# Kernel optimization log

Hardware: AMD Instinct MI355X
Metric: run time of the kernel (lower is better)

The kernel has to match this reference:

```python
import jax, jax.numpy as jnp
import numpy as np

TAU = 2.0      # spikingjelly MultiStepLIFNode default tau
VTH = 1.0      # default v_threshold
ALPHA = 4.0    # default Sigmoid surrogate alpha
EPS = 1e-5     # BatchNorm eps

# --- STE sign for binarized conv weights (Binarize.apply, det mode, scale=1) ---
@jax.custom_vjp
def ste_sign(x):
    return jnp.sign(x)

def _ss_fwd(x):
    return jnp.sign(x), None

def _ss_bwd(_, g):
    return (g,)

ste_sign.defvjp(_ss_fwd, _ss_bwd)

# --- Heaviside spike with sigmoid surrogate gradient ---
@jax.custom_vjp
def spike_fn(x):
    return (x >= 0.0).astype(x.dtype)

def _sp_fwd(x):
    return (x >= 0.0).astype(x.dtype), x

def _sp_bwd(x, g):
    s = jax.nn.sigmoid(ALPHA * x)
    return (g * ALPHA * s * (1.0 - s),)

spike_fn.defvjp(_sp_fwd, _sp_bwd)

def lif(x):
    # x: [T,B,C,H,W]; LIF with v_reset=None (soft reset), decay_input=True,
    # detach_reset=True (stop_gradient on the reset term).
    def step(v, xt):
        v = v + (xt - v) / TAU
        s = spike_fn(v - VTH)
        v = v - jax.lax.stop_gradient(s) * VTH
        return v, s
    v0 = jnp.zeros_like(x[0])
    _, spikes = jax.lax.scan(step, v0, x)
    return spikes

def conv3x3(x, w, groups=1):
    # x: [N,C,H,W], w: [O, C//groups, 3, 3], stride 1, pad 1
    return jax.lax.conv_general_dilated(
        x, w, window_strides=(1, 1), padding=((1, 1), (1, 1)),
        dimension_numbers=('NCHW', 'OIHW', 'NCHW'),
        feature_group_count=groups)

def setup_inputs() -> dict:
    key = jax.random.key(0)
    k1, k2, k3 = jax.random.split(key, 3)
    x = jax.random.normal(k1, (4, 8, 256, 64, 64), dtype=jnp.float32)
    w1 = jax.random.normal(k2, (192, 256, 3, 3), dtype=jnp.float32) * 0.05
    gamma = jnp.ones((192,), dtype=jnp.float32)
    beta = jnp.zeros((192,), dtype=jnp.float32)
    w2 = jax.random.normal(k3, (320, 48, 3, 3), dtype=jnp.float32) * 0.05
    return {'x': x, 'w1': w1, 'gamma': gamma, 'beta': beta, 'w2': w2}

def reference(x, w1, gamma, beta, w2):
    T, B, C, H, W = x.shape
    s = lif(x).reshape(T * B, C, H, W)          # spikes, flatten(0,1)
    y = conv3x3(s, w1)                          # conv1 (bias=False)
    # BatchNorm2d in training mode: batch stats over (N,H,W), biased var
    mean = y.mean(axis=(0, 2, 3))
    var = y.var(axis=(0, 2, 3))
    yb = (y - mean[None, :, None, None]) * jax.lax.rsqrt(var + EPS)[None, :, None, None]
    yb = yb * gamma[None, :, None, None] + beta[None, :, None, None]
    hidden = yb.shape[1]
    x1 = yb.reshape(T, B, hidden, H, W)
    z = conv3x3(yb, ste_sign(w2), groups=4)     # binarized-weight conv, groups=4
    x2 = z.reshape(T, B, -1, H, W)
    return jnp.concatenate((x1, x2), axis=2)    # [T,B,output_size,H,W]
```

## Files before the change

### kernel.cpp

```cpp
#include <hip/hip_runtime.h>

typedef __bf16 bf16x8 __attribute__((ext_vector_type(8)));
typedef float f32x4 __attribute__((ext_vector_type(4)));

#define DEV static __device__ __forceinline__

DEV ushort f2bf(float f) {
  unsigned u = __builtin_bit_cast(unsigned, f);
  u = (u + 0x7FFFu + ((u >> 16) & 1u)) >> 16;
  return (ushort)u;
}
DEV float bf2f(ushort h) {
  unsigned u = ((unsigned)h) << 16;
  return __builtin_bit_cast(float, u);
}
DEV void gll16(const void* g, void* l) {
  __builtin_amdgcn_global_load_lds((const __attribute__((address_space(1))) void*)g,
                                   (__attribute__((address_space(3))) void*)l, 16, 0, 0);
}

#define Y_OFF      71368704ull
#define WR1_OFF    121700352ull
#define WR2_OFF    122585088ull
#define STATS_OFF  122953728ull
#define ZERO_OFF   122955264ull
#define PART_OFF   122959360ull

DEV void border_px(int p, int& h, int& w) {
  if (p < 66)       { h = 0;       w = p; }
  else if (p < 132) { h = 65;      w = p - 66; }
  else if (p < 196) { h = p - 131; w = 0; }
  else              { h = p - 195; w = 65; }
}
__global__ void halo1_kernel(ushort* __restrict__ S) {
  const int idx = blockIdx.x * 256 + threadIdx.x;
  const int n = idx / 16640, r = idx % 16640;
  const int p = r >> 6, c4 = r & 63;
  int h, w; border_px(p, h, w);
  ushort4 z; z.x = 0; z.y = 0; z.z = 0; z.w = 0;
  *(ushort4*)&S[((size_t)((n * 66 + h) * 66 + w) << 8) + c4 * 4] = z;
}
__global__ void halo2_kernel(ushort* __restrict__ Yb) {
  const int idx = blockIdx.x * 256 + threadIdx.x;
  const int n = idx / 12480, r = idx % 12480;
  const int p = r / 48, c4 = r % 48;
  int h, w; border_px(p, h, w);
  ushort4 z; z.x = 0; z.y = 0; z.z = 0; z.w = 0;
  *(ushort4*)&Yb[(size_t)((n * 66 + h) * 66 + w) * 192 + c4 * 4] = z;
}

__global__ __launch_bounds__(256) void lif_kernel(const float* __restrict__ x,
                                                  ushort* __restrict__ S) {
  const int bi = blockIdx.x;
  const int jq = bi >> 9;
  const int b  = (bi >> 6) & 7;
  const int h  = bi & 63;
  const int tid = threadIdx.x;
  const int w0 = (tid & 15) << 2;
  const int cg = (tid >> 4) + (jq << 4);
  const int c0 = cg << 2;

  float v[4][4];
#pragma unroll
  for (int a = 0; a < 4; ++a)
#pragma unroll
    for (int k = 0; k < 4; ++k) v[a][k] = 0.f;

#pragma unroll
  for (int t = 0; t < 4; ++t) {
    const int n = t * 8 + b;
    ushort sp[4][4];
#pragma unroll
    for (int a = 0; a < 4; ++a) {
      const float4 xv = *(const float4*)(x + ((size_t)(n * 256 + c0 + a) << 12) + (h << 6) + w0);
      const float xa[4] = {xv.x, xv.y, xv.z, xv.w};
#pragma unroll
      for (int k = 0; k < 4; ++k) {
        v[a][k] += (xa[k] - v[a][k]) * 0.5f;
        const bool s = v[a][k] >= 1.0f;
        sp[a][k] = s ? (ushort)0x3F80 : (ushort)0;
        v[a][k] -= s ? 1.0f : 0.0f;
      }
    }
#pragma unroll
    for (int k = 0; k < 4; ++k) {
      ushort4 o4; o4.x = sp[0][k]; o4.y = sp[1][k]; o4.z = sp[2][k]; o4.w = sp[3][k];
      *(ushort4*)(S + ((size_t)((n * 66 + h + 1) * 66 + (w0 + k + 1)) << 8) + c0) = o4;
    }
  }
}

__global__ void prep_w1_kernel(const float* __restrict__ w1, ushort* __restrict__ Wr1) {
  const int idx = blockIdx.x * 256 + threadIdx.x;
  const int pos = idx / 49152, r = idx % 49152;
  const int o = r >> 8, c = r & 255;
  Wr1[idx] = f2bf(w1[(o * 256 + c) * 9 + pos]);
}
__global__ void prep_w2_kernel(const float* __restrict__ w2, ushort* __restrict__ Wr2) {
  const int idx = blockIdx.x * 256 + threadIdx.x;
  const int gp = idx / 5120, r = idx % 5120;
  const int o = r >> 6, c = r & 63;
  const int g = gp / 9, pos = gp % 9;
  float v = 0.f;
  if (c < 48) {
    const float wv = w2[((g * 80 + o) * 48 + c) * 9 + pos];
    v = (wv > 0.f) ? 1.f : ((wv < 0.f) ? -1.f : 0.f);
  }
  Wr2[idx] = f2bf(v);
}

__global__ __launch_bounds__(256, 2) void conv1_kernel(const ushort* __restrict__ S,
                                                       const ushort* __restrict__ Wr1,
                                                       ushort* __restrict__ Y,
                                                       float* __restrict__ Pp) {
  __shared__ ushort ldsA[2][12288];
  __shared__ ushort ldsB[2][8192];
  const int tid = threadIdx.x;
  const int l = tid & 63, wv = tid >> 6;
  const int wrow = wv >> 1, wcol = wv & 1;
  const int col = l & 15, quad = l >> 4;
  const int bid = ((blockIdx.x & 7) << 7) | (blockIdx.x >> 3);
  const int pxb = bid << 7;
  const int n = pxb >> 12;
  const int h0 = (pxb >> 6) & 63;
  const int n66h0 = n * 66 + h0;

  int goA[6], loA[6];
#pragma unroll
  for (int ii = 0; ii < 6; ++ii) {
    const int s = ii * 256 + tid;
    const int kc = s / 768, r = s % 768;
    const int row = r >> 2, op = r & 3;
    const int ol = (op - (row >> 1)) & 3;
    goA[ii] = row * 256 + kc * 32 + ol * 8;
    loA[ii] = s * 8;
  }
  int goB[4], loB[4];
#pragma unroll
  for (int ii = 0; ii < 4; ++ii) {
    const int s = ii * 256 + tid;
    const int kc = s >> 9, r = s & 511;
    const int pxl = r >> 2, op = r & 3;
    const int ol = (op - (pxl >> 1)) & 3;
    goB[ii] = ((pxl >> 6) * 66 + (pxl & 63)) * 256 + kc * 32 + ol * 8;
    loB[ii] = s * 8;
  }
  int offA[6], offB[4];
#pragma unroll
  for (int i = 0; i < 6; ++i) {
    const int row = wrow * 96 + i * 16 + col;
    offA[i] = row * 32 + (((quad + (row >> 1)) & 3) << 3);
  }
#pragma unroll
  for (int j = 0; j < 4; ++j) {
    const int row = wcol * 64 + j * 16 + col;
    offB[j] = row * 32 + (((quad + (row >> 1)) & 3) << 3);
  }

  f32x4 acc[6][4];
#pragma unroll
  for (int i = 0; i < 6; ++i)
#pragma unroll
    for (int j = 0; j < 4; ++j) acc[i][j] = (f32x4){0.f, 0.f, 0.f, 0.f};

  auto stage = [&](int it2, int buf) {
    const int pos = it2 >> 2, cc = it2 & 3;
    const int kh = pos / 3, kw = pos - 3 * kh;
    const int c0 = cc << 6;
    const int uA = pos * 49152 + c0;
    const int uB = ((n66h0 + kh) * 66 + kw) * 256 + c0;
#pragma unroll
    for (int ii = 0; ii < 6; ++ii)
      gll16(Wr1 + uA + goA[ii], &ldsA[buf][loA[ii]]);
#pragma unroll
    for (int ii = 0; ii < 4; ++ii)
      gll16(S + uB + goB[ii], &ldsB[buf][loB[ii]]);
  };

  auto computeTile = [&](int buf) {
#pragma unroll
    for (int kc = 0; kc < 2; ++kc) {
      bf16x8 bf[4];
#pragma unroll
      for (int j = 0; j < 4; ++j)
        bf[j] = *(const bf16x8*)&ldsB[buf][kc * 4096 + offB[j]];
#pragma unroll
      for (int i = 0; i < 6; ++i) {
        const bf16x8 af = *(const bf16x8*)&ldsA[buf][kc * 6144 + offA[i]];
#pragma unroll
        for (int j = 0; j < 4; ++j)
          acc[i][j] = __builtin_amdgcn_mfma_f32_16x16x32_bf16(af, bf[j], acc[i][j], 0, 0, 0);
      }
    }
  };

  stage(0, 0);
  __syncthreads();
  for (int it = 0; it < 36; it += 2) {
    stage(it + 1, 1);
    computeTile(0);
    __syncthreads();
    if (it + 2 < 36) stage(it + 2, 0);
    computeTile(1);
    __syncthreads();
  }

#pragma unroll
  for (int i = 0; i < 6; ++i) {
    const int o = wrow * 96 + i * 16 + quad * 4;
#pragma unroll
    for (int j = 0; j < 4; ++j) {
      const int px = pxb + wcol * 64 + j * 16 + col;
      ushort4 st;
      st.x = f2bf(acc[i][j].x); st.y = f2bf(acc[i][j].y);
      st.z = f2bf(acc[i][j].z); st.w = f2bf(acc[i][j].w);
      *(ushort4*)&Y[px * 192 + o] = st;
    }
  }
#pragma unroll
  for (int i = 0; i < 6; ++i) {
    float s[4], q[4];
#pragma unroll
    for (int k = 0; k < 4; ++k) { s[k] = 0.f; q[k] = 0.f; }
#pragma unroll
    for (int j = 0; j < 4; ++j)
#pragma unroll
      for (int k = 0; k < 4; ++k) {
        const float v = acc[i][j][k];
        s[k] += v; q[k] += v * v;
      }
#pragma unroll
    for (int m = 1; m < 16; m <<= 1)
#pragma unroll
      for (int k = 0; k < 4; ++k) {
        s[k] += __shfl_xor(s[k], m, 64);
        q[k] += __shfl_xor(q[k], m, 64);
      }
    if (col == 0) {
      const int oc = wrow * 96 + i * 16 + quad * 4;
      const int slot = (int)blockIdx.x * 2 + wcol;
#pragma unroll
      for (int k = 0; k < 4; ++k) {
        Pp[(oc + k) * 2048 + slot] = s[k];
        Pp[(192 + oc + k) * 2048 + slot] = q[k];
      }
    }
  }
}

__global__ void reduce_stats_kernel(const float* __restrict__ Pp, float* __restrict__ stats) {
  const int r = blockIdx.x, t = threadIdx.x;
  const float4 a = *(const float4*)&Pp[r * 2048 + t * 8];
  const float4 b = *(const float4*)&Pp[r * 2048 + t * 8 + 4];
  float s = a.x + a.y + a.z + a.w + b.x + b.y + b.z + b.w;
#pragma unroll
  for (int m = 32; m; m >>= 1) s += __shfl_xor(s, m, 64);
  __shared__ float ls[4];
  if ((t & 63) == 0) ls[t >> 6] = s;
  __syncthreads();
  if (t == 0) stats[r] = ls[0] + ls[1] + ls[2] + ls[3];
}

__global__ void bn_kernel(const ushort* __restrict__ Y, const float* __restrict__ stats,
                          const float* __restrict__ gamma, const float* __restrict__ beta,
                          float* __restrict__ out, ushort* __restrict__ Yb) {
  __shared__ float lds[13056];
  const int tid = threadIdx.x;
  const int n = blockIdx.x >> 6, h = blockIdx.x & 63;
  const int cq = tid % 48, wsub = tid / 48;
  const int c0 = cq * 4;
  float a[4], bb[4];
#pragma unroll
  for (int j = 0; j < 4; ++j) {
    const int c = c0 + j;
    const float mean = stats[c] * (1.f / 131072.f);
    const float var = stats[192 + c] * (1.f / 131072.f) - mean * mean;
    const float r = rsqrtf(var + 1e-5f);
    a[j] = gamma[c] * r;
    bb[j] = beta[c] - mean * a[j];
  }
  const int pxrow = n * 4096 + h * 64;
  for (int i = 0; i < 16; ++i) {
    const int w = i * 4 + wsub;
    const ushort4 yv = *(const ushort4*)&Y[(pxrow + w) * 192 + c0];
    float f[4];
    f[0] = a[0] * bf2f(yv.x) + bb[0];
    f[1] = a[1] * bf2f(yv.y) + bb[1];
    f[2] = a[2] * bf2f(yv.z) + bb[2];
    f[3] = a[3] * bf2f(yv.w) + bb[3];
    ushort4 ob;
    ob.x = f2bf(f[0]); ob.y = f2bf(f[1]); ob.z = f2bf(f[2]); ob.w = f2bf(f[3]);
    *(ushort4*)&Yb[(size_t)((n * 66 + h + 1) * 66 + (w + 1)) * 192 + c0] = ob;
#pragma unroll
    for (int j = 0; j < 4; ++j) lds[(c0 + j) * 68 + w] = f[j];
  }
  __syncthreads();
  const int w4 = (tid & 15) << 2, cz = tid >> 4;
  for (int i = 0; i < 16; ++i) {
    const int c = cz * 16 + i;
    const float4 v = *(const float4*)&lds[c * 68 + w4];
    *(float4*)&out[((size_t)(n * 512 + c) << 12) + h * 64 + w4] = v;
  }
}

__global__ __launch_bounds__(256, 2) void conv2_kernel(const ushort* __restrict__ Yb,
                                                       const ushort* __restrict__ Wr2,
                                                       const ushort* __restrict__ zb,
                                                       float* __restrict__ out) {
  __shared__ ushort ldsA[2][8192];
  __shared__ ushort ldsB[2][6144];
  const int tid = threadIdx.x;
  const int l = tid & 63, wv = tid >> 6;
  const int col = l & 15, quad = l >> 4;
  const int g = blockIdx.y;
  const int g48 = g * 48;
  const int bid = ((blockIdx.x & 7) << 7) | (blockIdx.x >> 3);
  const int pxb = bid << 7;
  const int n = pxb >> 12;
  const int h0 = (pxb >> 6) & 63;
  const int n66h0 = n * 66 + h0;

  int goA[4], loA[4];
  bool vA[4];
#pragma unroll
  for (int ii = 0; ii < 4; ++ii) {
    const int s = ii * 256 + tid;
    const int kc = s >> 9, r = s & 511;
    const int pxl = r >> 2, op = r & 3;
    const int ol = (op - (pxl >> 1)) & 3;
    const int c = kc * 32 + ol * 8;
    vA[ii] = (c < 48);
    goA[ii] = ((pxl >> 6) * 66 + (pxl & 63)) * 192 + c;
    loA[ii] = s * 8;
  }
  int gB[3], loB[3];
  bool vB[3];
#pragma unroll
  for (int ii = 0; ii < 3; ++ii) {
    const int s = ii * 256 + tid;
    const int kc = s / 384, r = s % 384;
    const int row = r >> 2, op = r & 3;
    const int ol = (op - (row >> 1)) & 3;
    vB[ii] = (row < 80);
    gB[ii] = row * 64 + kc * 32 + ol * 8;
    loB[ii] = s * 8;
  }
  int offA[2], offB[5];
#pragma unroll
  for (int i = 0; i < 2; ++i) {
    const int row = wv * 32 + i * 16 + col;
    offA[i] = row * 32 + (((quad + (row >> 1)) & 3) << 3);
  }
#pragma unroll
  for (int j = 0; j < 5; ++j) {
    const int row = j * 16 + col;
    offB[j] = row * 32 + (((quad + (row >> 1)) & 3) << 3);
  }

  f32x4 acc[2][5];
#pragma unroll
  for (int i = 0; i < 2; ++i)
#pragma unroll
    for (int j = 0; j < 5; ++j) acc[i][j] = (f32x4){0.f, 0.f, 0.f, 0.f};

  auto stage = [&](int pos, int buf) {
    const int kh = pos / 3, kw = pos - 3 * kh;
    const int uA = ((n66h0 + kh) * 66 + kw) * 192 + g48;
    const int wbase = (g * 9 + pos) * 5120;
#pragma unroll
    for (int ii = 0; ii < 4; ++ii) {
      const ushort* p = vA[ii] ? Yb + uA + goA[ii] : zb;
      gll16(p, &ldsA[buf][loA[ii]]);
    }
#pragma unroll
    for (int ii = 0; ii < 3; ++ii) {
      const ushort* p = vB[ii] ? Wr2 + wbase + gB[ii] : zb;
      gll16(p, &ldsB[buf][loB[ii]]);
    }
  };

  auto computeTile = [&](int buf) {
#pragma unroll
    for (int kc = 0; kc < 2; ++kc) {
      bf16x8 bw[5];
#pragma unroll
      for (int j = 0; j < 5; ++j)
        bw[j] = *(const bf16x8*)&ldsB[buf][kc * 3072 + offB[j]];
#pragma unroll
      for (int i = 0; i < 2; ++i) {
        const bf16x8 af = *(const bf16x8*)&ldsA[buf][kc * 4096 + offA[i]];
#pragma unroll
        for (int j = 0; j < 5; ++j)
          acc[i][j] = __builtin_amdgcn_mfma_f32_16x16x32_bf16(af, bw[j], acc[i][j], 0, 0, 0);
      }
    }
  };

  stage(0, 0);
  __syncthreads();
  for (int p = 0; p < 8; p += 2) {
    stage(p + 1, 1);
    computeTile(0);
    __syncthreads();
    stage(p + 2, 0);
    computeTile(1);
    __syncthreads();
  }
  computeTile(0);

#pragma unroll
  for (int i = 0; i < 2; ++i) {
    const int pxl = (pxb & 4095) + wv * 32 + i * 16 + quad * 4;
#pragma unroll
    for (int j = 0; j < 5; ++j) {
      const int o = 192 + g * 80 + j * 16 + col;
      float4 v4;
      v4.x = acc[i][j].x; v4.y = acc[i][j].y; v4.z = acc[i][j].z; v4.w = acc[i][j].w;
      *(float4*)&out[((size_t)(n * 512 + o) << 12) + pxl] = v4;
    }
  }
}

extern "C" void kernel_launch(void* const* d_in, const int* in_sizes, int n_in,
                              void* d_out, int out_size, void* d_ws, size_t ws_size,
                              hipStream_t stream) {
  const float* x     = (const float*)d_in[0];
  const float* w1    = (const float*)d_in[1];
  const float* gamma = (const float*)d_in[2];
  const float* beta  = (const float*)d_in[3];
  const float* w2    = (const float*)d_in[4];
  float* out = (float*)d_out;
  char* ws = (char*)d_ws;

  ushort* S   = (ushort*)ws;
  ushort* Yb  = (ushort*)ws;
  ushort* Y   = (ushort*)(ws + Y_OFF);
  ushort* Wr1 = (ushort*)(ws + WR1_OFF);
  ushort* Wr2 = (ushort*)(ws + WR2_OFF);
  float* stats = (float*)(ws + STATS_OFF);
  const ushort* zb = (const ushort*)(ws + ZERO_OFF);
  float* Pp = (float*)(ws + PART_OFF);

  hipMemsetAsync(ws + ZERO_OFF, 0, 4096, stream);
  hipLaunchKernelGGL(prep_w1_kernel, dim3(1728), dim3(256), 0, stream, w1, Wr1);
  hipLaunchKernelGGL(prep_w2_kernel, dim3(720), dim3(256), 0, stream, w2, Wr2);
  hipLaunchKernelGGL(halo1_kernel, dim3(2080), dim3(256), 0, stream, S);
  hipLaunchKernelGGL(lif_kernel, dim3(2048), dim3(256), 0, stream, x, S);
  hipLaunchKernelGGL(conv1_kernel, dim3(1024), dim3(256), 0, stream, S, Wr1, Y, Pp);
  hipLaunchKernelGGL(reduce_stats_kernel, dim3(384), dim3(256), 0, stream, Pp, stats);
  hipLaunchKernelGGL(halo2_kernel, dim3(1560), dim3(256), 0, stream, Yb);
  hipLaunchKernelGGL(bn_kernel, dim3(2048), dim3(192), 0, stream, Y, stats, gamma, beta, out, Yb);
  hipLaunchKernelGGL(conv2_kernel, dim3(1024, 4), dim3(256), 0, stream, Yb, Wr2, zb, out);
}
```

Measured before the change: 631.5 us.

## Deepen LDS prefetch pipeline with partial vmcnt waits in both conv GEMMs

Replaces the __syncthreads-based double buffering in both conv kernels with an explicit schedule. The kernel now keeps two stages of global_load_lds in flight and waits with s_waitcnt vmcnt(N) only for the older stage, using raw s_barrier and sched_barrier to stop compiler reordering. This lets global loads for the next tile overlap the MFMA work more fully instead of draining all memory operations at each barrier. The risk is correctness: the hardcoded vmcnt counts must match the number of loads each stage issues.

```diff
diff --git a/kernel.cpp b/kernel.cpp
--- a/kernel.cpp
+++ b/kernel.cpp
@@ -18,6 +18,10 @@
   __builtin_amdgcn_global_load_lds((const __attribute__((address_space(1))) void*)g,
                                    (__attribute__((address_space(3))) void*)l, 16, 0, 0);
 }
+
+#define WAITV(N) asm volatile("s_waitcnt vmcnt(" #N ")" ::: "memory")
+#define BAR __builtin_amdgcn_s_barrier()
+#define SCHED0 __builtin_amdgcn_sched_barrier(0)
 
 #define Y_OFF      71368704ull
 #define WR1_OFF    121700352ull
@@ -195,14 +199,19 @@
   };
 
   stage(0, 0);
-  __syncthreads();
+  stage(1, 1);
   for (int it = 0; it < 36; it += 2) {
-    stage(it + 1, 1);
+    WAITV(10); SCHED0;
+    BAR; SCHED0;
     computeTile(0);
-    __syncthreads();
+    BAR; SCHED0;
     if (it + 2 < 36) stage(it + 2, 0);
+    if (it + 3 < 36) { WAITV(10); } else { WAITV(0); }
+    SCHED0;
+    BAR; SCHED0;
     computeTile(1);
-    __syncthreads();
+    BAR; SCHED0;
+    if (it + 3 < 36) stage(it + 3, 1);
   }
 
 #pragma unroll
@@ -397,15 +406,21 @@
   };
 
   stage(0, 0);
-  __syncthreads();
+  stage(1, 1);
   for (int p = 0; p < 8; p += 2) {
-    stage(p + 1, 1);
+    WAITV(7); SCHED0;
+    BAR; SCHED0;
     computeTile(0);
-    __syncthreads();
-    stage(p + 2, 0);
+    BAR; SCHED0;
+    if (p + 2 < 9) stage(p + 2, 0);
+    if (p + 3 < 9) { WAITV(7); } else { WAITV(0); }
+    SCHED0;
+    BAR; SCHED0;
     computeTile(1);
-    __syncthreads();
-  }
+    BAR; SCHED0;
+    if (p + 3 < 9) stage(p + 3, 1);
+  }
+  BAR; SCHED0;
   computeTile(0);
 
 #pragma unroll
```

Measured after the change: 618.1 us. -2.1%, faster.
